# Kernel optimization log

Measured on AMD Instinct MI355X. Metric: run time of the kernel, lower is better.

## Reference

```python
import jax, jax.numpy as jnp
import numpy as np

# Config mirroring NEQUIPLayerFlax(hidden_irreps='64x0e + 64x1o', max_ell=1,
# avg_num_neighbors=16.0, num_species=5, mlp_n_hidden=64, mlp_n_layers=3, active_fn='relu')
N = 20000        # nodes
E = 320000       # edges (avg degree 16)
M = 64           # multiplicity per irrep
NR = 8           # radial embedding size
NSPEC = 5
AVG_NEI = 16.0
SQRT3 = 1.7320508075688772


def setup_inputs() -> dict:
    key = jax.random.key(0)
    ks = jax.random.split(key, 16)
    f32 = jnp.float32
    return {
        "vectors": jax.random.normal(ks[0], (E, 3), f32),
        "node_feats": jax.random.normal(ks[1], (N, 4 * M), f32),  # 64x0e (64) + 64x1o (192)
        "node_specie": jax.random.randint(ks[2], (N,), 0, NSPEC, jnp.int32),
        "radial_embedding": jax.random.uniform(ks[3], (E, NR), f32),
        "senders": jax.random.randint(ks[4], (E,), 0, N, jnp.int32),
        "receivers": jax.random.randint(ks[5], (E,), 0, N, jnp.int32),
        # linear_up: per-irrep-type mixing (no bias, e3nn-style /sqrt(fan_in))
        "W_up_s": jax.random.normal(ks[6], (M, M), f32),
        "W_up_v": jax.random.normal(ks[7], (M, M), f32),
        # radial MLP: NR -> 64 -> 64 -> 64 -> num_irreps(messages)=256
        "mlp_w1": jax.random.normal(ks[8], (NR, 64), f32),
        "mlp_w2": jax.random.normal(ks[9], (64, 64), f32),
        "mlp_w3": jax.random.normal(ks[10], (64, 64), f32),
        "mlp_wo": jax.random.normal(ks[11], (64, 4 * M), f32),
        # skip_tp: species-indexed linear node_feats -> (64x0e + 64x1o + 64x0e gates)
        "W_skip_s": jax.random.normal(ks[12], (NSPEC, M, 2 * M), f32),
        "W_skip_v": jax.random.normal(ks[13], (NSPEC, M, M), f32),
        # linear_down: messages (128x0e + 128x1o) -> (128x0e + 64x1o)
        "W_down_s": jax.random.normal(ks[14], (2 * M, 2 * M), f32),
        "W_down_v": jax.random.normal(ks[15], (2 * M, M), f32),
    }


def reference(vectors, node_feats, node_specie, radial_embedding, senders, receivers,
              W_up_s, W_up_v, mlp_w1, mlp_w2, mlp_w3, mlp_wo,
              W_skip_s, W_skip_v, W_down_s, W_down_v):
    n = node_feats.shape[0]
    s = node_feats[:, :M]                          # [N, 64]   0e
    v = node_feats[:, M:].reshape(n, M, 3)         # [N, 64,3] 1o

    inv_m = 1.0 / jnp.sqrt(jnp.asarray(M, node_feats.dtype))
    up_s = (s @ W_up_s) * inv_m                    # linear_up, scalar block
    up_v = jnp.einsum('nmc,mk->nkc', v, W_up_v) * inv_m

    es = up_s[senders]                             # [E, 64]
    ev = up_v[senders]                             # [E, 64, 3]

    # Y1 spherical harmonics, normalize=True, 'component' norm -> sqrt(3) * unit vector
    lengths = jnp.linalg.norm(vectors, axis=1, keepdims=True)         # [E,1]
    y = SQRT3 * vectors / lengths                                     # [E,3]

    # tensor products kept by filter_ir_out = hidden + '0e':
    # 1o x 1o -> 0e (CG = delta/sqrt(3), component norm)
    tp_s = jnp.einsum('emc,ec->em', ev, y) / SQRT3                    # [E,64]
    # 0e x 1o -> 1o (coefficient 1 under component norm)
    tp_v = es[:, :, None] * y[:, None, :]                             # [E,64,3]

    # concatenate + regroup -> 128x0e + 128x1o
    msg_s = jnp.concatenate([es, tp_s], axis=1)                       # [E,128]
    msg_v = jnp.concatenate([ev, tp_v], axis=1)                       # [E,128,3]

    # radial MLP (silu, /sqrt(fan_in) weight norm, no output activation)
    h = jax.nn.silu((radial_embedding @ mlp_w1) / jnp.sqrt(jnp.asarray(NR, jnp.float32)))
    h = jax.nn.silu((h @ mlp_w2) / 8.0)
    h = jax.nn.silu((h @ mlp_w3) / 8.0)
    mix = (h @ mlp_wo) / 8.0                                          # [E,256] = num_irreps
    mix = jnp.where(lengths == 0.0, 0.0, mix)

    msg_s = msg_s * mix[:, :2 * M]
    msg_v = msg_v * mix[:, 2 * M:, None]

    # scatter-sum to receivers, normalize by sqrt(avg_num_neighbors)
    inv_sq_nei = 1.0 / jnp.sqrt(jnp.asarray(AVG_NEI, jnp.float32))
    agg_s = jax.ops.segment_sum(msg_s, receivers, num_segments=n) * inv_sq_nei  # [N,128]
    agg_v = jax.ops.segment_sum(msg_v, receivers, num_segments=n) * inv_sq_nei  # [N,128,3]

    # linear_down -> irreps 64x0e + 64x1o + 64x0e(gates)  (scalars packed as 128)
    inv_2m = 1.0 / jnp.sqrt(jnp.asarray(2 * M, jnp.float32))
    down_s = (agg_s @ W_down_s) * inv_2m                              # [N,128]
    down_v = jnp.einsum('nmc,mk->nkc', agg_v, W_down_v) * inv_2m      # [N,64,3]

    # species-indexed skip connection from input node_feats
    Ws = W_skip_s[node_specie]                                        # [N,64,128]
    Wv = W_skip_v[node_specie]                                        # [N,64,64]
    skip_s = jnp.einsum('nm,nmk->nk', s, Ws) * inv_m                  # [N,128]
    skip_v = jnp.einsum('nmc,nmk->nkc', v, Wv) * inv_m                # [N,64,3]

    f_s = down_s + skip_s
    f_v = down_v + skip_v

    # gate: first 64 scalars are features (even_act=silu), last 64 scalars gate the 1o's
    gated_s = jax.nn.silu(f_s[:, :M])                                 # [N,64]
    gates = jax.nn.silu(f_s[:, M:])                                   # [N,64]
    gated_v = gates[:, :, None] * f_v                                 # [N,64,3]

    out = jnp.concatenate([gated_s, gated_v.reshape(n, 3 * M)], axis=1)  # [N,256]
    return jax.nn.relu(out)  # active_fn == 'relu'
```

## Files before the change

kernel.cpp:

```cpp
#include <hip/hip_runtime.h>
#include <hip/hip_fp16.h>

#define NN 20000
#define EE 320000
#define BCAP3 64

typedef _Float16 f16;
typedef f16  f16x8 __attribute__((ext_vector_type(8)));
typedef float f32x4 __attribute__((ext_vector_type(4)));

__device__ __forceinline__ float silu_f(float x) {
    return x / (1.0f + __expf(-x));
}

__global__ __launch_bounds__(256) void up_kernel(
    const float* __restrict__ nf, const float* __restrict__ Wus,
    const float* __restrict__ Wuv, float* __restrict__ up, int dmajor)
{
    __shared__ float sWs[64 * 64];
    __shared__ float sWv[64 * 64];
    int tid = threadIdx.x;
    for (int i = tid; i < 64 * 64; i += 256) { sWs[i] = Wus[i]; sWv[i] = Wuv[i]; }
    __syncthreads();
    int lane = tid & 63, wv = tid >> 6;
    for (int it = 0; it < 4; it++) {
        int n = blockIdx.x * 16 + wv * 4 + it;
        const float* row = nf + (size_t)n * 256;
        float s  = row[lane];
        float v0 = row[64 + lane * 3 + 0];
        float v1 = row[64 + lane * 3 + 1];
        float v2 = row[64 + lane * 3 + 2];
        float as = 0.f, a0 = 0.f, a1 = 0.f, a2 = 0.f;
        #pragma unroll 8
        for (int m = 0; m < 64; m++) {
            float sm = __shfl(s, m);
            float b0 = __shfl(v0, m), b1 = __shfl(v1, m), b2 = __shfl(v2, m);
            float w_s = sWs[m * 64 + lane];
            float w_v = sWv[m * 64 + lane];
            as += sm * w_s;
            a0 += b0 * w_v; a1 += b1 * w_v; a2 += b2 * w_v;
        }
        float* o = up + (size_t)n * 256;
        if (dmajor) {
            o[lane]       = as * 0.125f;
            o[64  + lane] = a0 * 0.125f;
            o[128 + lane] = a1 * 0.125f;
            o[192 + lane] = a2 * 0.125f;
        } else {
            o[lane] = as * 0.125f;
            o[64 + lane * 3 + 0] = a0 * 0.125f;
            o[64 + lane * 3 + 1] = a1 * 0.125f;
            o[64 + lane * 3 + 2] = a2 * 0.125f;
        }
    }
}

__global__ __launch_bounds__(256) void pack_kernel(
    const float* __restrict__ w1, const float* __restrict__ w2,
    const float* __restrict__ w3, const float* __restrict__ wo,
    f16* __restrict__ wp)
{
    int idx = blockIdx.x * 256 + threadIdx.x;
    if (idx >= 52 * 64) return;
    int frag = idx >> 6, lane = idx & 63;
    int col = lane & 15, kg = lane >> 4;
    f16x8 pv;
    if (frag < 4) {
        int t = frag;
        #pragma unroll
        for (int i = 0; i < 8; i++) {
            int k = kg * 8 + i;
            pv[i] = (k < 8) ? (f16)w1[k * 64 + t * 16 + col] : (f16)0.f;
        }
    } else if (frag < 12) {
        int f = frag - 4, t = f >> 1, h = f & 1;
        #pragma unroll
        for (int i = 0; i < 8; i++) {
            int k = h * 32 + kg * 8 + i;
            pv[i] = (f16)w2[k * 64 + t * 16 + col];
        }
    } else if (frag < 20) {
        int f = frag - 12, t = f >> 1, h = f & 1;
        #pragma unroll
        for (int i = 0; i < 8; i++) {
            int k = h * 32 + kg * 8 + i;
            pv[i] = (f16)w3[k * 64 + t * 16 + col];
        }
    } else {
        int f = frag - 20, t = f >> 1, h = f & 1;
        #pragma unroll
        for (int i = 0; i < 8; i++) {
            int k = h * 32 + kg * 8 + i;
            pv[i] = (f16)wo[k * 256 + t * 16 + col];
        }
    }
    *(f16x8*)(wp + (size_t)idx * 8) = pv;
}

__global__ __launch_bounds__(256) void pack2_kernel(
    const float* __restrict__ Wds, const float* __restrict__ Wdv,
    const float* __restrict__ Wss, const float* __restrict__ Wsv,
    f16* __restrict__ wp2)
{
    int idx = blockIdx.x * 256 + threadIdx.x;
    if (idx >= 168 * 64) return;
    int frag = idx >> 6, lane = idx & 63;
    int col = lane & 15, kg = lane >> 4;
    const float S_d = 0.25f * 0.08838834764831845f;
    const float S_k = 0.125f;
    f16x8 pv;
    if (frag < 32) {
        int t = frag >> 2, kf = frag & 3;
        #pragma unroll
        for (int i = 0; i < 8; i++) {
            int k = kf * 32 + kg * 8 + i;
            pv[i] = (f16)(Wds[k * 128 + t * 16 + col] * S_d);
        }
    } else if (frag < 48) {
        int f = frag - 32; int t = f >> 2, kf = f & 3;
        #pragma unroll
        for (int i = 0; i < 8; i++) {
            int k = kf * 32 + kg * 8 + i;
            pv[i] = (f16)(Wdv[k * 64 + t * 16 + col] * S_d);
        }
    } else if (frag < 128) {
        int f = frag - 48; int sp = f >> 4; int t = (f & 15) >> 1; int kf = f & 1;
        #pragma unroll
        for (int i = 0; i < 8; i++) {
            int k = kf * 32 + kg * 8 + i;
            pv[i] = (f16)(Wss[((size_t)sp * 64 + k) * 128 + t * 16 + col] * S_k);
        }
    } else {
        int f = frag - 128; int sp = f >> 3; int t = (f & 7) >> 1; int kf = f & 1;
        #pragma unroll
        for (int i = 0; i < 8; i++) {
            int k = kf * 32 + kg * 8 + i;
            pv[i] = (f16)(Wsv[((size_t)sp * 64 + k) * 64 + t * 16 + col] * S_k);
        }
    }
    *(f16x8*)(wp2 + (size_t)idx * 8) = pv;
}

__global__ void bucket_kernel(const int* __restrict__ rcv,
                              const int* __restrict__ snd,
                              int* __restrict__ cnt, int2* __restrict__ list)
{
    int e = blockIdx.x * 256 + threadIdx.x;
    int r = rcv[e];
    if ((unsigned)r >= (unsigned)NN) return;
    int s = snd[e];
    int pos = atomicAdd(&cnt[r], 1);
    if (pos < BCAP3) list[(size_t)r * BCAP3 + pos] = make_int2(e, s);
}

__global__ __launch_bounds__(256) void mlp_mix(
    const float* __restrict__ radial, const f16* __restrict__ wp,
    f16* __restrict__ mix)
{
    __shared__ f16 smem[4 * 6144];
    int tid = threadIdx.x, lane = tid & 63, w = tid >> 6;
    f16* actA = smem + w * 6144;
    f16* actB = actA + 1024;
    f16* outT = actB + 1024;
    int e0 = (blockIdx.x * 4 + w) * 16;

    int col = lane & 15;
    int kg  = lane >> 4;
    const f32x4 zero = {0.f, 0.f, 0.f, 0.f};

    #define LDB(fr) (*(const f16x8*)(wp + ((size_t)(fr) * 64 + lane) * 8))
    #define LDA(buf, h) (*(const f16x8*)((buf) + (lane & 15) * 64 + \
                        (((kg * 8) + (h) * 32) ^ (((lane & 15) & 7) << 3))))
    #define STACT(buf, acc, SC)                                            \
        _Pragma("unroll")                                                  \
        for (int t = 0; t < 4; t++) {                                      \
            _Pragma("unroll")                                              \
            for (int r = 0; r < 4; r++) {                                  \
                int row = kg * 4 + r;                                      \
                int c   = t * 16 + col;                                    \
                float x = acc[t][r] * (SC);                                \
                (buf)[row * 64 + (c ^ ((row & 7) << 3))] = (f16)silu_f(x); \
            }                                                              \
        }

    {
        f16x8 a;
        if (lane < 16) {
            const float* rr = radial + (size_t)(e0 + lane) * 8;
            float4 ra = *(const float4*)rr;
            float4 rb = *(const float4*)(rr + 4);
            a[0] = (f16)ra.x; a[1] = (f16)ra.y; a[2] = (f16)ra.z; a[3] = (f16)ra.w;
            a[4] = (f16)rb.x; a[5] = (f16)rb.y; a[6] = (f16)rb.z; a[7] = (f16)rb.w;
        } else {
            #pragma unroll
            for (int i = 0; i < 8; i++) a[i] = (f16)0.f;
        }
        f32x4 acc[4];
        #pragma unroll
        for (int t = 0; t < 4; t++)
            acc[t] = __builtin_amdgcn_mfma_f32_16x16x32_f16(a, LDB(t), zero, 0, 0, 0);
        STACT(actA, acc, 0.35355339059327373f)
    }
    {
        f16x8 a0 = LDA(actA, 0), a1 = LDA(actA, 1);
        f32x4 acc[4];
        #pragma unroll
        for (int t = 0; t < 4; t++) {
            acc[t] = __builtin_amdgcn_mfma_f32_16x16x32_f16(a0, LDB(4 + t * 2), zero, 0, 0, 0);
            acc[t] = __builtin_amdgcn_mfma_f32_16x16x32_f16(a1, LDB(5 + t * 2), acc[t], 0, 0, 0);
        }
        STACT(actB, acc, 0.125f)
    }
    {
        f16x8 a0 = LDA(actB, 0), a1 = LDA(actB, 1);
        f32x4 acc[4];
        #pragma unroll
        for (int t = 0; t < 4; t++) {
            acc[t] = __builtin_amdgcn_mfma_f32_16x16x32_f16(a0, LDB(12 + t * 2), zero, 0, 0, 0);
            acc[t] = __builtin_amdgcn_mfma_f32_16x16x32_f16(a1, LDB(13 + t * 2), acc[t], 0, 0, 0);
        }
        STACT(actA, acc, 0.125f)
    }
    {
        f16x8 a0 = LDA(actA, 0), a1 = LDA(actA, 1);
        #pragma unroll
        for (int tg = 0; tg < 4; tg++) {
            f32x4 acc[4];
            #pragma unroll
            for (int q = 0; q < 4; q++) {
                int t = tg * 4 + q;
                acc[q] = __builtin_amdgcn_mfma_f32_16x16x32_f16(a0, LDB(20 + t * 2), zero, 0, 0, 0);
                acc[q] = __builtin_amdgcn_mfma_f32_16x16x32_f16(a1, LDB(21 + t * 2), acc[q], 0, 0, 0);
            }
            #pragma unroll
            for (int q = 0; q < 4; q++) {
                int t = tg * 4 + q;
                #pragma unroll
                for (int r = 0; r < 4; r++) {
                    int row = kg * 4 + r;
                    int c   = t * 16 + col;
                    outT[row * 256 + (c ^ ((row & 7) << 3))] = (f16)(acc[q][r] * 0.125f);
                }
            }
        }
    }
    #pragma unroll
    for (int j = 0; j < 8; j++) {
        int li  = j * 64 + lane;
        int row = li >> 5;
        int ci  = (li & 31) * 8;
        f16x8 v = *(const f16x8*)(outT + row * 256 + (ci ^ ((row & 7) << 3)));
        *(f16x8*)(mix + (size_t)(e0 + row) * 256 + ci) = v;
    }
    #undef LDB
    #undef LDA
    #undef STACT
}

__global__ __launch_bounds__(256) void gather_kernel(
    const float* __restrict__ vectors,
    const f16* __restrict__ mix, const float* __restrict__ up2,
    const int* __restrict__ cnt, const int2* __restrict__ list,
    f16* __restrict__ agg)
{
    int tid = threadIdx.x, lane = tid & 63, w = tid >> 6;
    int n = blockIdx.x * 4 + w;
    if ((unsigned)n >= (unsigned)NN) return;
    int count = cnt[n];
    if (count > BCAP3) count = BCAP3;
    if (count < 0) count = 0;

    int sec = lane >> 3;
    int m0  = (lane & 7) * 8;
    int upoff = (sec == 2) ? 64 + m0 : (sec == 3) ? 128 + m0
              : (sec == 4) ? 192 + m0 : m0;
    int mq = (sec == 0) ? 0 : (sec == 1) ? 64 : (sec <= 4) ? 128 : 192;
    const float SQ3 = 1.7320508075688772f;

    float a0=0,a1=0,a2=0,a3=0,a4=0,a5=0,a6=0,a7=0;
    const int2* mylist = list + (size_t)n * BCAP3;

    for (int k = 0; k < count; k++) {
        int2 es = mylist[k];
        int e   = es.x;
        int snd = es.y;
        if ((unsigned)e >= (unsigned)EE) e = 0;
        if ((unsigned)snd >= (unsigned)NN) snd = 0;
        float vx = vectors[(size_t)e * 3 + 0];
        float vy = vectors[(size_t)e * 3 + 1];
        float vz = vectors[(size_t)e * 3 + 2];
        float l2 = vx * vx + vy * vy + vz * vz;
        float il   = (l2 > 0.f) ? rsqrtf(l2) : 0.f;
        float mask = (l2 > 0.f) ? 1.f : 0.f;

        f16x8 mv = *(const f16x8*)(mix + (size_t)e * 256 + mq + m0);
        const float* u = up2 + (size_t)snd * 256;

        if (sec != 1) {
            float g = (sec == 5) ? SQ3 * vx * il
                    : (sec == 6) ? SQ3 * vy * il
                    : (sec == 7) ? SQ3 * vz * il : mask;
            const float* ub = u + upoff;
            float4 u0 = *(const float4*)(ub);
            float4 u1 = *(const float4*)(ub + 4);
            a0 += u0.x * g * (float)mv[0];
            a1 += u0.y * g * (float)mv[1];
            a2 += u0.z * g * (float)mv[2];
            a3 += u0.w * g * (float)mv[3];
            a4 += u1.x * g * (float)mv[4];
            a5 += u1.y * g * (float)mv[5];
            a6 += u1.z * g * (float)mv[6];
            a7 += u1.w * g * (float)mv[7];
        } else {
            float4 ex0 = *(const float4*)(u + 64  + m0);
            float4 ex1 = *(const float4*)(u + 64  + m0 + 4);
            float4 ey0 = *(const float4*)(u + 128 + m0);
            float4 ey1 = *(const float4*)(u + 128 + m0 + 4);
            float4 ez0 = *(const float4*)(u + 192 + m0);
            float4 ez1 = *(const float4*)(u + 192 + m0 + 4);
            a0 += (ex0.x * vx + ey0.x * vy + ez0.x * vz) * il * (float)mv[0];
            a1 += (ex0.y * vx + ey0.y * vy + ez0.y * vz) * il * (float)mv[1];
            a2 += (ex0.z * vx + ey0.z * vy + ez0.z * vz) * il * (float)mv[2];
            a3 += (ex0.w * vx + ey0.w * vy + ez0.w * vz) * il * (float)mv[3];
            a4 += (ex1.x * vx + ey1.x * vy + ez1.x * vz) * il * (float)mv[4];
            a5 += (ex1.y * vx + ey1.y * vy + ez1.y * vz) * il * (float)mv[5];
            a6 += (ex1.z * vx + ey1.z * vy + ez1.z * vz) * il * (float)mv[6];
            a7 += (ex1.w * vx + ey1.w * vy + ez1.w * vz) * il * (float)mv[7];
        }
    }
    f16x8 o;
    o[0] = (f16)a0; o[1] = (f16)a1; o[2] = (f16)a2; o[3] = (f16)a3;
    o[4] = (f16)a4; o[5] = (f16)a5; o[6] = (f16)a6; o[7] = (f16)a7;
    *(f16x8*)(agg + (size_t)n * 512 + lane * 8) = o;
}

__global__ __launch_bounds__(256) void node_mfma(
    const float* __restrict__ nf, const int* __restrict__ specie,
    const f16* __restrict__ wp2, const f16* __restrict__ agg,
    float* __restrict__ out)
{
    int tid = threadIdx.x, lane = tid & 63, w = tid >> 6;
    int n0 = (blockIdx.x * 4 + w) * 16;
    if (n0 >= NN) return;
    int col = lane & 15, kg = lane >> 4;
    int myn = n0 + col;
    int mysp = specie[myn];
    if ((unsigned)mysp >= 5u) mysp = 0;
    const f32x4 zero = {0.f, 0.f, 0.f, 0.f};
    const f16x8 zv = {};

    #define LDB2(fr) (*(const f16x8*)(wp2 + ((size_t)(fr) * 64 + lane) * 8))

    f32x4 accs[8];
    #pragma unroll
    for (int t = 0; t < 8; t++) accs[t] = zero;
    #pragma unroll
    for (int kf = 0; kf < 4; kf++) {
        f16x8 a = *(const f16x8*)(agg + (size_t)myn * 512 + kf * 32 + kg * 8);
        #pragma unroll
        for (int t = 0; t < 8; t++)
            accs[t] = __builtin_amdgcn_mfma_f32_16x16x32_f16(a, LDB2(t * 4 + kf), accs[t], 0, 0, 0);
    }
    #pragma unroll
    for (int kf = 0; kf < 2; kf++) {
        const float* base = nf + (size_t)myn * 256 + kf * 32 + kg * 8;
        float4 x0 = *(const float4*)(base);
        float4 x1 = *(const float4*)(base + 4);
        f16x8 a;
        a[0] = (f16)x0.x; a[1] = (f16)x0.y; a[2] = (f16)x0.z; a[3] = (f16)x0.w;
        a[4] = (f16)x1.x; a[5] = (f16)x1.y; a[6] = (f16)x1.z; a[7] = (f16)x1.w;
        #pragma unroll
        for (int sp = 0; sp < 5; sp++) {
            f16x8 am = (mysp == sp) ? a : zv;
            #pragma unroll
            for (int t = 0; t < 8; t++)
                accs[t] = __builtin_amdgcn_mfma_f32_16x16x32_f16(am, LDB2(48 + sp * 16 + t * 2 + kf), accs[t], 0, 0, 0);
        }
    }
    float gates[4][4];
    #pragma unroll
    for (int t = 0; t < 4; t++) {
        #pragma unroll
        for (int r = 0; r < 4; r++) {
            int n = n0 + kg * 4 + r;
            out[(size_t)n * 256 + t * 16 + col] = fmaxf(silu_f(accs[t][r]), 0.f);
            gates[t][r] = silu_f(accs[4 + t][r]);
        }
    }

    #pragma unroll
    for (int c = 0; c < 3; c++) {
        f32x4 accv[4];
        #pragma unroll
        for (int t = 0; t < 4; t++) accv[t] = zero;
        #pragma unroll
        for (int kf = 0; kf < 4; kf++) {
            int off = (kf < 2) ? (128 + c * 64 + kf * 32) : (320 + c * 64 + (kf - 2) * 32);
            f16x8 a = *(const f16x8*)(agg + (size_t)myn * 512 + off + kg * 8);
            #pragma unroll
            for (int t = 0; t < 4; t++)
                accv[t] = __builtin_amdgcn_mfma_f32_16x16x32_f16(a, LDB2(32 + t * 4 + kf), accv[t], 0, 0, 0);
        }
        #pragma unroll
        for (int kf = 0; kf < 2; kf++) {
            const float* base = nf + (size_t)myn * 256 + 64 + (kf * 32 + kg * 8) * 3;
            float4 q0 = *(const float4*)(base);
            float4 q1 = *(const float4*)(base + 4);
            float4 q2 = *(const float4*)(base + 8);
            float4 q3 = *(const float4*)(base + 12);
            float4 q4 = *(const float4*)(base + 16);
            float4 q5 = *(const float4*)(base + 20);
            float qa[24] = {q0.x, q0.y, q0.z, q0.w, q1.x, q1.y, q1.z, q1.w,
                            q2.x, q2.y, q2.z, q2.w, q3.x, q3.y, q3.z, q3.w,
                            q4.x, q4.y, q4.z, q4.w, q5.x, q5.y, q5.z, q5.w};
            f16x8 a;
            #pragma unroll
            for (int i = 0; i < 8; i++) a[i] = (f16)qa[i * 3 + c];
            #pragma unroll
            for (int sp = 0; sp < 5; sp++) {
                f16x8 am = (mysp == sp) ? a : zv;
                #pragma unroll
                for (int t = 0; t < 4; t++)
                    accv[t] = __builtin_amdgcn_mfma_f32_16x16x32_f16(am, LDB2(128 + sp * 8 + t * 2 + kf), accv[t], 0, 0, 0);
            }
        }
        #pragma unroll
        for (int t = 0; t < 4; t++) {
            #pragma unroll
            for (int r = 0; r < 4; r++) {
                int n = n0 + kg * 4 + r;
                out[(size_t)n * 256 + 64 + (t * 16 + col) * 3 + c] =
                    fmaxf(gates[t][r] * accv[t][r], 0.f);
            }
        }
    }
    #undef LDB2
}

__global__ __launch_bounds__(256) void node_kernel_f(
    const float* __restrict__ nf, const int* __restrict__ specie,
    const float* __restrict__ Wds, const float* __restrict__ Wdv,
    const float* __restrict__ Wss, const float* __restrict__ Wsv,
    const float* __restrict__ agg, float* __restrict__ out)
{
    __shared__ float sDs[128 * 128];
    __shared__ float sDv[128 * 64];
    int tid = threadIdx.x;
    for (int i = tid; i < 128 * 128; i += 256) sDs[i] = Wds[i];
    for (int i = tid; i < 128 * 64; i += 256) sDv[i] = Wdv[i];
    __syncthreads();
    int lane = tid & 63, wv = tid >> 6;
    for (int it = 0; it < 4; it++) {
        int n = blockIdx.x * 16 + wv * 4 + it;
        const float* arow = agg + (size_t)n * 512;
        const float inv_nei = 0.25f;
        float as0 = arow[lane] * inv_nei;
        float as1 = arow[64 + lane] * inv_nei;
        float av00 = arow[128 + lane] * inv_nei;
        float av01 = arow[192 + lane] * inv_nei;
        float av02 = arow[256 + lane] * inv_nei;
        float av10 = arow[320 + lane] * inv_nei;
        float av11 = arow[384 + lane] * inv_nei;
        float av12 = arow[448 + lane] * inv_nei;
        const float* row = nf + (size_t)n * 256;
        float s   = row[lane];
        float vv0 = row[64 + lane * 3 + 0];
        float vv1 = row[64 + lane * 3 + 1];
        float vv2 = row[64 + lane * 3 + 2];

        float f0 = 0.f, f1 = 0.f, fv0 = 0.f, fv1 = 0.f, fv2 = 0.f;
        #pragma unroll 8
        for (int m = 0; m < 64; m++) {
            float am = __shfl(as0, m);
            f0 += am * sDs[m * 128 + lane];
            f1 += am * sDs[m * 128 + 64 + lane];
            float b0 = __shfl(av00, m), b1 = __shfl(av01, m), b2 = __shfl(av02, m);
            float wd = sDv[m * 64 + lane];
            fv0 += b0 * wd; fv1 += b1 * wd; fv2 += b2 * wd;
        }
        #pragma unroll 8
        for (int m = 0; m < 64; m++) {
            float am = __shfl(as1, m);
            f0 += am * sDs[(64 + m) * 128 + lane];
            f1 += am * sDs[(64 + m) * 128 + 64 + lane];
            float b0 = __shfl(av10, m), b1 = __shfl(av11, m), b2 = __shfl(av12, m);
            float wd = sDv[(64 + m) * 64 + lane];
            fv0 += b0 * wd; fv1 += b1 * wd; fv2 += b2 * wd;
        }
        const float inv2m = 0.08838834764831845f;
        f0 *= inv2m; f1 *= inv2m; fv0 *= inv2m; fv1 *= inv2m; fv2 *= inv2m;

        int sp = specie[n];
        if ((unsigned)sp >= 5u) sp = 0;
        const float* Ws = Wss + (size_t)sp * 64 * 128;
        const float* Wv = Wsv + (size_t)sp * 64 * 64;
        float g0 = 0.f, g1 = 0.f, h0 = 0.f, h1 = 0.f, h2 = 0.f;
        #pragma unroll 4
        for (int m = 0; m < 64; m++) {
            float sm = __shfl(s, m);
            g0 += sm * Ws[m * 128 + lane];
            g1 += sm * Ws[m * 128 + 64 + lane];
            float b0 = __shfl(vv0, m), b1 = __shfl(vv1, m), b2 = __shfl(vv2, m);
            float wsk = Wv[m * 64 + lane];
            h0 += b0 * wsk; h1 += b1 * wsk; h2 += b2 * wsk;
        }
        f0 += g0 * 0.125f; f1 += g1 * 0.125f;
        fv0 += h0 * 0.125f; fv1 += h1 * 0.125f; fv2 += h2 * 0.125f;

        float gs   = silu_f(f0);
        float gate = silu_f(f1);
        float* orow = out + (size_t)n * 256;
        orow[lane] = fmaxf(gs, 0.f);
        orow[64 + lane * 3 + 0] = fmaxf(gate * fv0, 0.f);
        orow[64 + lane * 3 + 1] = fmaxf(gate * fv1, 0.f);
        orow[64 + lane * 3 + 2] = fmaxf(gate * fv2, 0.f);
    }
}

__global__ __launch_bounds__(256) void edge_kernel_fb(
    const float* __restrict__ vectors, const float* __restrict__ radial,
    const int* __restrict__ senders, const int* __restrict__ receivers,
    const float* __restrict__ w1, const float* __restrict__ w2,
    const float* __restrict__ w3, const float* __restrict__ wo,
    const float* __restrict__ up, float* __restrict__ agg)
{
    __shared__ __half2 hL[32 * 256];
    __shared__ float   T[16 * 256];
    __shared__ float   sVec[256 * 3];
    __shared__ int     sSnd[256];
    __shared__ int     sRcv[256];

    int tid = threadIdx.x;
    int e = blockIdx.x * 256 + tid;
    int snd = senders[e];
    int rcv = receivers[e];
    if ((unsigned)snd >= (unsigned)NN) snd = 0;
    if ((unsigned)rcv >= (unsigned)NN) rcv = 0;
    float4 ra = *(const float4*)(radial + (size_t)e * 8);
    float4 rb = *(const float4*)(radial + (size_t)e * 8 + 4);
    float vx = vectors[(size_t)e * 3 + 0];
    float vy = vectors[(size_t)e * 3 + 1];
    float vz = vectors[(size_t)e * 3 + 2];
    sSnd[tid] = snd; sRcv[tid] = rcv;
    sVec[tid * 3 + 0] = vx; sVec[tid * 3 + 1] = vy; sVec[tid * 3 + 2] = vz;
    float len2 = vx * vx + vy * vy + vz * vz;
    float mask = (len2 > 0.f) ? 1.f : 0.f;

    {
        float a[64];
        #pragma unroll
        for (int j = 0; j < 64; j++) {
            float acc = ra.x * w1[j]       + ra.y * w1[64 + j]
                      + ra.z * w1[128 + j] + ra.w * w1[192 + j]
                      + rb.x * w1[256 + j] + rb.y * w1[320 + j]
                      + rb.z * w1[384 + j] + rb.w * w1[448 + j];
            a[j] = silu_f(acc * 0.35355339059327373f);
        }
        #pragma unroll
        for (int jp = 0; jp < 32; jp++)
            hL[jp * 256 + tid] = __floats2half2_rn(a[2 * jp], a[2 * jp + 1]);
    }
    {
        float acc[64];
        #pragma unroll
        for (int j = 0; j < 64; j++) acc[j] = 0.f;
        #pragma unroll 2
        for (int kp = 0; kp < 32; kp++) {
            float2 hf = __half22float2(hL[kp * 256 + tid]);
            const float* wr0 = w2 + (size_t)(2 * kp) * 64;
            const float* wr1 = w2 + (size_t)(2 * kp + 1) * 64;
            #pragma unroll
            for (int j = 0; j < 64; j++) acc[j] += hf.x * wr0[j] + hf.y * wr1[j];
        }
        #pragma unroll
        for (int jp = 0; jp < 32; jp++)
            hL[jp * 256 + tid] = __floats2half2_rn(silu_f(acc[2 * jp] * 0.125f),
                                                   silu_f(acc[2 * jp + 1] * 0.125f));
    }
    {
        float acc[64];
        #pragma unroll
        for (int j = 0; j < 64; j++) acc[j] = 0.f;
        #pragma unroll 2
        for (int kp = 0; kp < 32; kp++) {
            float2 hf = __half22float2(hL[kp * 256 + tid]);
            const float* wr0 = w3 + (size_t)(2 * kp) * 64;
            const float* wr1 = w3 + (size_t)(2 * kp + 1) * 64;
            #pragma unroll
            for (int j = 0; j < 64; j++) acc[j] += hf.x * wr0[j] + hf.y * wr1[j];
        }
        #pragma unroll
        for (int jp = 0; jp < 32; jp++)
            hL[jp * 256 + tid] = __floats2half2_rn(silu_f(acc[2 * jp] * 0.125f),
                                                   silu_f(acc[2 * jp + 1] * 0.125f));
    }

    int lane  = tid & 63;
    int wbase = tid & 192;
    int f = lane & 15;
    int g = lane >> 4;

    #define COMPUTE_CHUNK(c, ao)                                                \
        {                                                                       \
            _Pragma("unroll")                                                   \
            for (int j = 0; j < 16; j++) ao[j] = 0.f;                           \
            _Pragma("unroll 4")                                                 \
            for (int kp = 0; kp < 32; kp++) {                                   \
                float2 hf = __half22float2(hL[kp * 256 + tid]);                 \
                const float* wr0 = wo + (size_t)(2 * kp) * 256 + (c) * 16;      \
                const float* wr1 = wo + (size_t)(2 * kp + 1) * 256 + (c) * 16;  \
                _Pragma("unroll")                                               \
                for (int j = 0; j < 16; j++)                                    \
                    ao[j] += hf.x * wr0[j] + hf.y * wr1[j];                     \
            }                                                                   \
            _Pragma("unroll")                                                   \
            for (int j = 0; j < 16; j++) ao[j] *= 0.125f * mask;                \
        }

    #define WRITE_T(ao)                                                         \
        __syncthreads();                                                        \
        _Pragma("unroll")                                                       \
        for (int j = 0; j < 16; j++) T[j * 256 + (tid ^ (2 * j))] = ao[j];      \
        __syncthreads();

    for (int c = 0; c < 4; c++) {
        float ao[16];
        COMPUTE_CHUNK(c, ao)
        WRITE_T(ao)
        for (int el = 0; el < 16; el++) {
            int col = wbase + el * 4 + g;
            int s_ = sSnd[col], rc = sRcv[col];
            float mx = T[f * 256 + (col ^ (2 * f))];
            int jf = c * 16 + f;
            atomicAdd(agg + (size_t)rc * 512 + jf, up[(size_t)s_ * 256 + jf] * mx);
        }
    }
    for (int c = 4; c < 8; c++) {
        float ao[16];
        COMPUTE_CHUNK(c, ao)
        WRITE_T(ao)
        for (int el = 0; el < 16; el++) {
            int col = wbase + el * 4 + g;
            int s_ = sSnd[col], rc = sRcv[col];
            float wx = sVec[col * 3 + 0], wy = sVec[col * 3 + 1], wz = sVec[col * 3 + 2];
            float l2 = wx * wx + wy * wy + wz * wz;
            float il = (l2 > 0.f) ? rsqrtf(l2) : 0.f;
            float mx = T[f * 256 + (col ^ (2 * f))];
            int m = (c - 4) * 16 + f;
            const float* ev = up + (size_t)s_ * 256 + 64 + m * 3;
            float dot = ev[0] * wx + ev[1] * wy + ev[2] * wz;
            atomicAdd(agg + (size_t)rc * 512 + 64 + m, dot * il * mx);
        }
    }
    for (int c = 8; c < 12; c++) {
        float ao[16];
        COMPUTE_CHUNK(c, ao)
        WRITE_T(ao)
        for (int el = 0; el < 16; el++) {
            int col = wbase + el * 4 + g;
            int s_ = sSnd[col], rc = sRcv[col];
            float mx = T[f * 256 + (col ^ (2 * f))];
            int m = (c - 8) * 16 + f;
            const float* ev = up + (size_t)s_ * 256 + 64 + m * 3;
            float* ag = agg + (size_t)rc * 512 + 128 + m;
            atomicAdd(ag + 0,   ev[0] * mx);
            atomicAdd(ag + 64,  ev[1] * mx);
            atomicAdd(ag + 128, ev[2] * mx);
        }
    }
    for (int c = 12; c < 16; c++) {
        float ao[16];
        COMPUTE_CHUNK(c, ao)
        WRITE_T(ao)
        for (int el = 0; el < 16; el++) {
            int col = wbase + el * 4 + g;
            int s_ = sSnd[col], rc = sRcv[col];
            float wx = sVec[col * 3 + 0], wy = sVec[col * 3 + 1], wz = sVec[col * 3 + 2];
            float l2 = wx * wx + wy * wy + wz * wz;
            float il = (l2 > 0.f) ? rsqrtf(l2) : 0.f;
            float mx = T[f * 256 + (col ^ (2 * f))];
            int m = (c - 12) * 16 + f;
            float sc = up[(size_t)s_ * 256 + m] * 1.7320508075688772f * il * mx;
            float* ag = agg + (size_t)rc * 512 + 320 + m;
            atomicAdd(ag + 0,   sc * wx);
            atomicAdd(ag + 64,  sc * wy);
            atomicAdd(ag + 128, sc * wz);
        }
    }
    #undef COMPUTE_CHUNK
    #undef WRITE_T
}

extern "C" void kernel_launch(void* const* d_in, const int* in_sizes, int n_in,
                              void* d_out, int out_size, void* d_ws, size_t ws_size,
                              hipStream_t stream) {
    const float* vectors     = (const float*)d_in[0];
    const float* node_feats  = (const float*)d_in[1];
    const int*   node_specie = (const int*)d_in[2];
    const float* radial      = (const float*)d_in[3];
    const int*   senders     = (const int*)d_in[4];
    const int*   receivers   = (const int*)d_in[5];
    const float* W_up_s      = (const float*)d_in[6];
    const float* W_up_v      = (const float*)d_in[7];
    const float* mlp_w1      = (const float*)d_in[8];
    const float* mlp_w2      = (const float*)d_in[9];
    const float* mlp_w3      = (const float*)d_in[10];
    const float* mlp_wo      = (const float*)d_in[11];
    const float* W_skip_s    = (const float*)d_in[12];
    const float* W_skip_v    = (const float*)d_in[13];
    const float* W_down_s    = (const float*)d_in[14];
    const float* W_down_v    = (const float*)d_in[15];
    float* out = (float*)d_out;

    float* up   = (float*)d_ws;
    float* aggf = up + (size_t)NN * 256;
    f16*   aggh = (f16*)aggf;
    int*   cnt  = (int*)((char*)aggf + 21 * 1024 * 1024);
    int2*  list = (int2*)(cnt + 20480);
    uintptr_t wp_addr = ((uintptr_t)(aggf + (size_t)NN * 512) + 255) & ~(uintptr_t)255;
    f16* wpack = (f16*)wp_addr;
    f16* wp2   = wpack + (size_t)52 * 64 * 8;
    uintptr_t mix_addr = ((uintptr_t)(wp2 + (size_t)168 * 64 * 8) + 255) & ~(uintptr_t)255;
    f16* mix = (f16*)mix_addr;
    size_t required = (size_t)(mix_addr + (size_t)EE * 256 * sizeof(f16)
                               - (uintptr_t)d_ws);

    if (ws_size >= required) {
        hipMemsetAsync(cnt, 0, NN * sizeof(int), stream);
        pack_kernel<<<13, 256, 0, stream>>>(mlp_w1, mlp_w2, mlp_w3, mlp_wo, wpack);
        pack2_kernel<<<42, 256, 0, stream>>>(W_down_s, W_down_v, W_skip_s, W_skip_v, wp2);
        up_kernel<<<NN / 16, 256, 0, stream>>>(node_feats, W_up_s, W_up_v, up, 1);
        bucket_kernel<<<EE / 256, 256, 0, stream>>>(receivers, senders, cnt, list);
        mlp_mix<<<EE / 64, 256, 0, stream>>>(radial, wpack, mix);
        gather_kernel<<<NN / 4, 256, 0, stream>>>(vectors, mix, up,
            cnt, list, aggh);
        node_mfma<<<(NN / 16 + 3) / 4, 256, 0, stream>>>(node_feats, node_specie,
            wp2, aggh, out);
    } else {
        hipMemsetAsync(aggf, 0, (size_t)NN * 512 * sizeof(float), stream);
        up_kernel<<<NN / 16, 256, 0, stream>>>(node_feats, W_up_s, W_up_v, up, 0);
        edge_kernel_fb<<<EE / 256, 256, 0, stream>>>(
            vectors, radial, senders, receivers,
            mlp_w1, mlp_w2, mlp_w3, mlp_wo, up, aggf);
        node_kernel_f<<<NN / 16, 256, 0, stream>>>(node_feats, node_specie,
            W_down_s, W_down_v, W_skip_s, W_skip_v, aggf, out);
    }
}
```

Baseline: 324.2 us.

## Sort edges by receiver via CSR scan so gather reads mix contiguously

Adds a prefix-sum over per-receiver counts and a slot-map kernel that produces receiver-sorted edge order, then runs the edge MLP in that order so the per-edge mix rows for each node are stored contiguously. The gather kernel reads its messages sequentially instead of from scattered edge rows, improving locality on the large fp16 mix buffer. It adds a single-block scan and a scatter kernel, and moves the random access to the small radial rows.

```diff
diff --git a/kernel.cpp b/kernel.cpp
--- a/kernel.cpp
+++ b/kernel.cpp
@@ -153,16 +153,58 @@
     if (pos < BCAP3) list[(size_t)r * BCAP3 + pos] = make_int2(e, s);
 }
 
+__global__ __launch_bounds__(256) void scan_kernel(
+    const int* __restrict__ cnt, int* __restrict__ off)
+{
+    __shared__ int partial[256];
+    int t = threadIdx.x;
+    int base = t * 79;
+    int end  = base + 79; if (end > NN) end = NN; if (base > NN) base = NN;
+    int sum = 0;
+    for (int i = base; i < end; i++) {
+        int c = cnt[i]; if (c > BCAP3) c = BCAP3; if (c < 0) c = 0;
+        sum += c;
+    }
+    partial[t] = sum;
+    __syncthreads();
+    for (int d = 1; d < 256; d <<= 1) {
+        int v = (t >= d) ? partial[t - d] : 0;
+        __syncthreads();
+        partial[t] += v;
+        __syncthreads();
+    }
+    int run = (t == 0) ? 0 : partial[t - 1];
+    for (int i = base; i < end; i++) {
+        int c = cnt[i]; if (c > BCAP3) c = BCAP3; if (c < 0) c = 0;
+        off[i] = run;
+        run += c;
+    }
+}
+
+__global__ __launch_bounds__(256) void slotmap_kernel(
+    const int* __restrict__ cnt, const int* __restrict__ off,
+    const int2* __restrict__ list, int2* __restrict__ slotEs)
+{
+    int idx = blockIdx.x * 256 + threadIdx.x;
+    int n = idx >> 6, k = idx & 63;
+    if (n >= NN) return;
+    int c = cnt[n]; if (c > BCAP3) c = BCAP3; if (c < 0) c = 0;
+    if (k >= c) return;
+    int pos = off[n] + k;
+    if ((unsigned)pos < (unsigned)EE)
+        slotEs[pos] = list[(size_t)n * BCAP3 + k];
+}
+
 __global__ __launch_bounds__(256) void mlp_mix(
     const float* __restrict__ radial, const f16* __restrict__ wp,
-    f16* __restrict__ mix)
+    const int2* __restrict__ slotEs, f16* __restrict__ mix)
 {
     __shared__ f16 smem[4 * 6144];
     int tid = threadIdx.x, lane = tid & 63, w = tid >> 6;
     f16* actA = smem + w * 6144;
     f16* actB = actA + 1024;
     f16* outT = actB + 1024;
-    int e0 = (blockIdx.x * 4 + w) * 16;
+    int s0 = (blockIdx.x * 4 + w) * 16;
 
     int col = lane & 15;
     int kg  = lane >> 4;
@@ -186,7 +228,9 @@
     {
         f16x8 a;
         if (lane < 16) {
-            const float* rr = radial + (size_t)(e0 + lane) * 8;
+            int e = slotEs[s0 + lane].x;
+            if ((unsigned)e >= (unsigned)EE) e = 0;
+            const float* rr = radial + (size_t)e * 8;
             float4 ra = *(const float4*)rr;
             float4 rb = *(const float4*)(rr + 4);
             a[0] = (f16)ra.x; a[1] = (f16)ra.y; a[2] = (f16)ra.z; a[3] = (f16)ra.w;
@@ -250,7 +294,7 @@
         int row = li >> 5;
         int ci  = (li & 31) * 8;
         f16x8 v = *(const f16x8*)(outT + row * 256 + (ci ^ ((row & 7) << 3)));
-        *(f16x8*)(mix + (size_t)(e0 + row) * 256 + ci) = v;
+        *(f16x8*)(mix + (size_t)(s0 + row) * 256 + ci) = v;
     }
     #undef LDB
     #undef LDA
@@ -260,8 +304,8 @@
 __global__ __launch_bounds__(256) void gather_kernel(
     const float* __restrict__ vectors,
     const f16* __restrict__ mix, const float* __restrict__ up2,
-    const int* __restrict__ cnt, const int2* __restrict__ list,
-    f16* __restrict__ agg)
+    const int* __restrict__ cnt, const int* __restrict__ off,
+    const int2* __restrict__ slotEs, f16* __restrict__ agg)
 {
     int tid = threadIdx.x, lane = tid & 63, w = tid >> 6;
     int n = blockIdx.x * 4 + w;
@@ -269,6 +313,10 @@
     int count = cnt[n];
     if (count > BCAP3) count = BCAP3;
     if (count < 0) count = 0;
+    int o = off[n];
+    if (o < 0) o = 0;
+    if (o > EE) o = EE;
+    if (o + count > EE) count = EE - o;
 
     int sec = lane >> 3;
     int m0  = (lane & 7) * 8;
@@ -278,7 +326,8 @@
     const float SQ3 = 1.7320508075688772f;
 
     float a0=0,a1=0,a2=0,a3=0,a4=0,a5=0,a6=0,a7=0;
-    const int2* mylist = list + (size_t)n * BCAP3;
+    const int2* mylist = slotEs + o;
+    const f16*  mybase = mix + (size_t)o * 256;
 
     for (int k = 0; k < count; k++) {
         int2 es = mylist[k];
@@ -293,7 +342,7 @@
         float il   = (l2 > 0.f) ? rsqrtf(l2) : 0.f;
         float mask = (l2 > 0.f) ? 1.f : 0.f;
 
-        f16x8 mv = *(const f16x8*)(mix + (size_t)e * 256 + mq + m0);
+        f16x8 mv = *(const f16x8*)(mybase + (size_t)k * 256 + mq + m0);
         const float* u = up2 + (size_t)snd * 256;
 
         if (sec != 1) {
@@ -328,10 +377,10 @@
             a7 += (ex1.w * vx + ey1.w * vy + ez1.w * vz) * il * (float)mv[7];
         }
     }
-    f16x8 o;
-    o[0] = (f16)a0; o[1] = (f16)a1; o[2] = (f16)a2; o[3] = (f16)a3;
-    o[4] = (f16)a4; o[5] = (f16)a5; o[6] = (f16)a6; o[7] = (f16)a7;
-    *(f16x8*)(agg + (size_t)n * 512 + lane * 8) = o;
+    f16x8 oo;
+    oo[0] = (f16)a0; oo[1] = (f16)a1; oo[2] = (f16)a2; oo[3] = (f16)a3;
+    oo[4] = (f16)a4; oo[5] = (f16)a5; oo[6] = (f16)a6; oo[7] = (f16)a7;
+    *(f16x8*)(agg + (size_t)n * 512 + lane * 8) = oo;
 }
 
 __global__ __launch_bounds__(256) void node_mfma(
@@ -395,8 +444,8 @@
         for (int t = 0; t < 4; t++) accv[t] = zero;
         #pragma unroll
         for (int kf = 0; kf < 4; kf++) {
-            int off = (kf < 2) ? (128 + c * 64 + kf * 32) : (320 + c * 64 + (kf - 2) * 32);
-            f16x8 a = *(const f16x8*)(agg + (size_t)myn * 512 + off + kg * 8);
+            int off2 = (kf < 2) ? (128 + c * 64 + kf * 32) : (320 + c * 64 + (kf - 2) * 32);
+            f16x8 a = *(const f16x8*)(agg + (size_t)myn * 512 + off2 + kg * 8);
             #pragma unroll
             for (int t = 0; t < 4; t++)
                 accv[t] = __builtin_amdgcn_mfma_f32_16x16x32_f16(a, LDB2(32 + t * 4 + kf), accv[t], 0, 0, 0);
@@ -716,7 +765,9 @@
     float* aggf = up + (size_t)NN * 256;
     f16*   aggh = (f16*)aggf;
     int*   cnt  = (int*)((char*)aggf + 21 * 1024 * 1024);
-    int2*  list = (int2*)(cnt + 20480);
+    int*   offs = cnt + 20480;
+    int2*  slotEs = (int2*)(offs + 20480);
+    int2*  list = slotEs + EE;
     uintptr_t wp_addr = ((uintptr_t)(aggf + (size_t)NN * 512) + 255) & ~(uintptr_t)255;
     f16* wpack = (f16*)wp_addr;
     f16* wp2   = wpack + (size_t)52 * 64 * 8;
@@ -731,9 +782,11 @@
         pack2_kernel<<<42, 256, 0, stream>>>(W_down_s, W_down_v, W_skip_s, W_skip_v, wp2);
         up_kernel<<<NN / 16, 256, 0, stream>>>(node_feats, W_up_s, W_up_v, up, 1);
         bucket_kernel<<<EE / 256, 256, 0, stream>>>(receivers, senders, cnt, list);
-        mlp_mix<<<EE / 64, 256, 0, stream>>>(radial, wpack, mix);
+        scan_kernel<<<1, 256, 0, stream>>>(cnt, offs);
+        slotmap_kernel<<<NN * 64 / 256, 256, 0, stream>>>(cnt, offs, list, slotEs);
+        mlp_mix<<<EE / 64, 256, 0, stream>>>(radial, wpack, slotEs, mix);
         gather_kernel<<<NN / 4, 256, 0, stream>>>(vectors, mix, up,
-            cnt, list, aggh);
+            cnt, offs, slotEs, aggh);
         node_mfma<<<(NN / 16 + 3) / 4, 256, 0, stream>>>(node_feats, node_specie,
             wp2, aggh, out);
     } else {
```

Result: slower. 367.7 us (+13.4%).

## Fuse radial MLP into per-receiver gather, drop edge mix buffer

Applied to the files above, without the earlier changes.

Merges the per-edge radial MLP kernel and the receiver gather kernel into one. Each wavefront now takes up to 16 of its node's incoming edges at a time, runs the MLP on them with MFMA, keeps the 256-wide mixing weights in shared memory, and accumulates messages straight from there. This removes writing and re-reading the E×256 fp16 mix buffer, about 160MB of traffic each way. In exchange, MLP tiles are only partly filled when a node has fewer than 16 or an awkward number of neighbours, and the edge-wise MLP is now serialised with the gather inside each wave.

```diff
diff --git a/kernel.cpp b/kernel.cpp
--- a/kernel.cpp
+++ b/kernel.cpp
@@ -153,185 +153,177 @@
     if (pos < BCAP3) list[(size_t)r * BCAP3 + pos] = make_int2(e, s);
 }
 
-__global__ __launch_bounds__(256) void mlp_mix(
+__global__ __launch_bounds__(256) void mlp_gather2(
     const float* __restrict__ radial, const f16* __restrict__ wp,
-    f16* __restrict__ mix)
+    const float* __restrict__ vectors, const float* __restrict__ up2,
+    const int* __restrict__ cnt, const int2* __restrict__ list,
+    f16* __restrict__ agg)
 {
-    __shared__ f16 smem[4 * 6144];
+    __shared__ f16 smem[4 * 5120];
     int tid = threadIdx.x, lane = tid & 63, w = tid >> 6;
-    f16* actA = smem + w * 6144;
-    f16* actB = actA + 1024;
-    f16* outT = actB + 1024;
-    int e0 = (blockIdx.x * 4 + w) * 16;
-
-    int col = lane & 15;
-    int kg  = lane >> 4;
+    f16* actA = smem + w * 5120;
+    f16* outT = actA + 1024;
+    int n = blockIdx.x * 4 + w;
+    if ((unsigned)n >= (unsigned)NN) return;
+    int count = cnt[n];
+    if (count > BCAP3) count = BCAP3;
+    if (count < 0) count = 0;
+
+    int col = lane & 15, kg = lane >> 4;
     const f32x4 zero = {0.f, 0.f, 0.f, 0.f};
+    const float SQ3 = 1.7320508075688772f;
+
+    int sec = lane >> 3;
+    int m0  = (lane & 7) * 8;
+    int upoff = (sec == 2) ? 64 + m0 : (sec == 3) ? 128 + m0
+              : (sec == 4) ? 192 + m0 : m0;
+    int mq = (sec == 0) ? 0 : (sec == 1) ? 64 : (sec <= 4) ? 128 : 192;
+    float a0=0,a1=0,a2=0,a3=0,a4=0,a5=0,a6=0,a7=0;
+
+    const int2* mylist = list + (size_t)n * BCAP3;
 
     #define LDB(fr) (*(const f16x8*)(wp + ((size_t)(fr) * 64 + lane) * 8))
     #define LDA(buf, h) (*(const f16x8*)((buf) + (lane & 15) * 64 + \
                         (((kg * 8) + (h) * 32) ^ (((lane & 15) & 7) << 3))))
-    #define STACT(buf, acc, SC)                                            \
+    #define STACT(buf, a4v, SC)                                            \
         _Pragma("unroll")                                                  \
         for (int t = 0; t < 4; t++) {                                      \
             _Pragma("unroll")                                              \
             for (int r = 0; r < 4; r++) {                                  \
                 int row = kg * 4 + r;                                      \
                 int c   = t * 16 + col;                                    \
-                float x = acc[t][r] * (SC);                                \
+                float x = a4v[t][r] * (SC);                                \
                 (buf)[row * 64 + (c ^ ((row & 7) << 3))] = (f16)silu_f(x); \
             }                                                              \
         }
 
-    {
-        f16x8 a;
-        if (lane < 16) {
-            const float* rr = radial + (size_t)(e0 + lane) * 8;
-            float4 ra = *(const float4*)rr;
-            float4 rb = *(const float4*)(rr + 4);
-            a[0] = (f16)ra.x; a[1] = (f16)ra.y; a[2] = (f16)ra.z; a[3] = (f16)ra.w;
-            a[4] = (f16)rb.x; a[5] = (f16)rb.y; a[6] = (f16)rb.z; a[7] = (f16)rb.w;
-        } else {
-            #pragma unroll
-            for (int i = 0; i < 8; i++) a[i] = (f16)0.f;
-        }
-        f32x4 acc[4];
-        #pragma unroll
-        for (int t = 0; t < 4; t++)
-            acc[t] = __builtin_amdgcn_mfma_f32_16x16x32_f16(a, LDB(t), zero, 0, 0, 0);
-        STACT(actA, acc, 0.35355339059327373f)
-    }
-    {
-        f16x8 a0 = LDA(actA, 0), a1 = LDA(actA, 1);
-        f32x4 acc[4];
-        #pragma unroll
-        for (int t = 0; t < 4; t++) {
-            acc[t] = __builtin_amdgcn_mfma_f32_16x16x32_f16(a0, LDB(4 + t * 2), zero, 0, 0, 0);
-            acc[t] = __builtin_amdgcn_mfma_f32_16x16x32_f16(a1, LDB(5 + t * 2), acc[t], 0, 0, 0);
-        }
-        STACT(actB, acc, 0.125f)
-    }
-    {
-        f16x8 a0 = LDA(actB, 0), a1 = LDA(actB, 1);
-        f32x4 acc[4];
-        #pragma unroll
-        for (int t = 0; t < 4; t++) {
-            acc[t] = __builtin_amdgcn_mfma_f32_16x16x32_f16(a0, LDB(12 + t * 2), zero, 0, 0, 0);
-            acc[t] = __builtin_amdgcn_mfma_f32_16x16x32_f16(a1, LDB(13 + t * 2), acc[t], 0, 0, 0);
-        }
-        STACT(actA, acc, 0.125f)
-    }
-    {
-        f16x8 a0 = LDA(actA, 0), a1 = LDA(actA, 1);
-        #pragma unroll
-        for (int tg = 0; tg < 4; tg++) {
-            f32x4 acc[4];
-            #pragma unroll
-            for (int q = 0; q < 4; q++) {
-                int t = tg * 4 + q;
-                acc[q] = __builtin_amdgcn_mfma_f32_16x16x32_f16(a0, LDB(20 + t * 2), zero, 0, 0, 0);
-                acc[q] = __builtin_amdgcn_mfma_f32_16x16x32_f16(a1, LDB(21 + t * 2), acc[q], 0, 0, 0);
+    for (int base = 0; base < count; base += 16) {
+        int2 es = make_int2(0, 0);
+        bool valid = (lane < 16) && (base + lane < count);
+        if (valid) es = mylist[base + lane];
+
+        {
+            f16x8 a;
+            if (valid) {
+                int e = es.x;
+                if ((unsigned)e >= (unsigned)EE) e = 0;
+                const float* rr = radial + (size_t)e * 8;
+                float4 ra = *(const float4*)rr;
+                float4 rb = *(const float4*)(rr + 4);
+                a[0] = (f16)ra.x; a[1] = (f16)ra.y; a[2] = (f16)ra.z; a[3] = (f16)ra.w;
+                a[4] = (f16)rb.x; a[5] = (f16)rb.y; a[6] = (f16)rb.z; a[7] = (f16)rb.w;
+            } else {
+                #pragma unroll
+                for (int i = 0; i < 8; i++) a[i] = (f16)0.f;
             }
-            #pragma unroll
-            for (int q = 0; q < 4; q++) {
-                int t = tg * 4 + q;
+            f32x4 av[4];
+            #pragma unroll
+            for (int t = 0; t < 4; t++)
+                av[t] = __builtin_amdgcn_mfma_f32_16x16x32_f16(a, LDB(t), zero, 0, 0, 0);
+            STACT(actA, av, 0.35355339059327373f)
+        }
+        {
+            f16x8 q0 = LDA(actA, 0), q1 = LDA(actA, 1);
+            f32x4 av[4];
+            #pragma unroll
+            for (int t = 0; t < 4; t++) {
+                av[t] = __builtin_amdgcn_mfma_f32_16x16x32_f16(q0, LDB(4 + t * 2), zero, 0, 0, 0);
+                av[t] = __builtin_amdgcn_mfma_f32_16x16x32_f16(q1, LDB(5 + t * 2), av[t], 0, 0, 0);
+            }
+            STACT(actA, av, 0.125f)
+        }
+        {
+            f16x8 q0 = LDA(actA, 0), q1 = LDA(actA, 1);
+            f32x4 av[4];
+            #pragma unroll
+            for (int t = 0; t < 4; t++) {
+                av[t] = __builtin_amdgcn_mfma_f32_16x16x32_f16(q0, LDB(12 + t * 2), zero, 0, 0, 0);
+                av[t] = __builtin_amdgcn_mfma_f32_16x16x32_f16(q1, LDB(13 + t * 2), av[t], 0, 0, 0);
+            }
+            STACT(actA, av, 0.125f)
+        }
+        {
+            f16x8 q0 = LDA(actA, 0), q1 = LDA(actA, 1);
+            #pragma unroll
+            for (int tg = 0; tg < 4; tg++) {
+                f32x4 av[4];
                 #pragma unroll
-                for (int r = 0; r < 4; r++) {
-                    int row = kg * 4 + r;
-                    int c   = t * 16 + col;
-                    outT[row * 256 + (c ^ ((row & 7) << 3))] = (f16)(acc[q][r] * 0.125f);
+                for (int q = 0; q < 4; q++) {
+                    int t = tg * 4 + q;
+                    av[q] = __builtin_amdgcn_mfma_f32_16x16x32_f16(q0, LDB(20 + t * 2), zero, 0, 0, 0);
+                    av[q] = __builtin_amdgcn_mfma_f32_16x16x32_f16(q1, LDB(21 + t * 2), av[q], 0, 0, 0);
+                }
+                #pragma unroll
+                for (int q = 0; q < 4; q++) {
+                    int t = tg * 4 + q;
+                    #pragma unroll
+                    for (int r = 0; r < 4; r++) {
+                        int row = kg * 4 + r;
+                        int c   = t * 16 + col;
+                        outT[row * 256 + (c ^ ((row & 7) << 3))] = (f16)(av[q][r] * 0.125f);
+                    }
                 }
             }
         }
-    }
-    #pragma unroll
-    for (int j = 0; j < 8; j++) {
-        int li  = j * 64 + lane;
-        int row = li >> 5;
-        int ci  = (li & 31) * 8;
-        f16x8 v = *(const f16x8*)(outT + row * 256 + (ci ^ ((row & 7) << 3)));
-        *(f16x8*)(mix + (size_t)(e0 + row) * 256 + ci) = v;
+
+        int nel = count - base; if (nel > 16) nel = 16;
+        for (int el = 0; el < nel; el++) {
+            int e   = __shfl(es.x, el);
+            int snd = __shfl(es.y, el);
+            if ((unsigned)e >= (unsigned)EE) e = 0;
+            if ((unsigned)snd >= (unsigned)NN) snd = 0;
+            float vx = vectors[(size_t)e * 3 + 0];
+            float vy = vectors[(size_t)e * 3 + 1];
+            float vz = vectors[(size_t)e * 3 + 2];
+            float l2 = vx * vx + vy * vy + vz * vz;
+            float il   = (l2 > 0.f) ? rsqrtf(l2) : 0.f;
+            float mask = (l2 > 0.f) ? 1.f : 0.f;
+
+            int sw = (el & 7) << 3;
+            f16x8 mv = *(const f16x8*)(outT + el * 256 + ((mq + m0) ^ sw));
+            const float* u = up2 + (size_t)snd * 256;
+
+            if (sec != 1) {
+                float g = (sec == 5) ? SQ3 * vx * il
+                        : (sec == 6) ? SQ3 * vy * il
+                        : (sec == 7) ? SQ3 * vz * il : mask;
+                const float* ub = u + upoff;
+                float4 u0 = *(const float4*)(ub);
+                float4 u1 = *(const float4*)(ub + 4);
+                a0 += u0.x * g * (float)mv[0];
+                a1 += u0.y * g * (float)mv[1];
+                a2 += u0.z * g * (float)mv[2];
+                a3 += u0.w * g * (float)mv[3];
+                a4 += u1.x * g * (float)mv[4];
+                a5 += u1.y * g * (float)mv[5];
+                a6 += u1.z * g * (float)mv[6];
+                a7 += u1.w * g * (float)mv[7];
+            } else {
+                float4 ex0 = *(const float4*)(u + 64  + m0);
+                float4 ex1 = *(const float4*)(u + 64  + m0 + 4);
+                float4 ey0 = *(const float4*)(u + 128 + m0);
+                float4 ey1 = *(const float4*)(u + 128 + m0 + 4);
+                float4 ez0 = *(const float4*)(u + 192 + m0);
+                float4 ez1 = *(const float4*)(u + 192 + m0 + 4);
+                a0 += (ex0.x * vx + ey0.x * vy + ez0.x * vz) * il * (float)mv[0];
+                a1 += (ex0.y * vx + ey0.y * vy + ez0.y * vz) * il * (float)mv[1];
+                a2 += (ex0.z * vx + ey0.z * vy + ez0.z * vz) * il * (float)mv[2];
+                a3 += (ex0.w * vx + ey0.w * vy + ez0.w * vz) * il * (float)mv[3];
+                a4 += (ex1.x * vx + ey1.x * vy + ez1.x * vz) * il * (float)mv[4];
+                a5 += (ex1.y * vx + ey1.y * vy + ez1.y * vz) * il * (float)mv[5];
+                a6 += (ex1.z * vx + ey1.z * vy + ez1.z * vz) * il * (float)mv[6];
+                a7 += (ex1.w * vx + ey1.w * vy + ez1.w * vz) * il * (float)mv[7];
+            }
+        }
     }
     #undef LDB
     #undef LDA
     #undef STACT
-}
-
-__global__ __launch_bounds__(256) void gather_kernel(
-    const float* __restrict__ vectors,
-    const f16* __restrict__ mix, const float* __restrict__ up2,
-    const int* __restrict__ cnt, const int2* __restrict__ list,
-    f16* __restrict__ agg)
-{
-    int tid = threadIdx.x, lane = tid & 63, w = tid >> 6;
-    int n = blockIdx.x * 4 + w;
-    if ((unsigned)n >= (unsigned)NN) return;
-    int count = cnt[n];
-    if (count > BCAP3) count = BCAP3;
-    if (count < 0) count = 0;
-
-    int sec = lane >> 3;
-    int m0  = (lane & 7) * 8;
-    int upoff = (sec == 2) ? 64 + m0 : (sec == 3) ? 128 + m0
-              : (sec == 4) ? 192 + m0 : m0;
-    int mq = (sec == 0) ? 0 : (sec == 1) ? 64 : (sec <= 4) ? 128 : 192;
-    const float SQ3 = 1.7320508075688772f;
-
-    float a0=0,a1=0,a2=0,a3=0,a4=0,a5=0,a6=0,a7=0;
-    const int2* mylist = list + (size_t)n * BCAP3;
-
-    for (int k = 0; k < count; k++) {
-        int2 es = mylist[k];
-        int e   = es.x;
-        int snd = es.y;
-        if ((unsigned)e >= (unsigned)EE) e = 0;
-        if ((unsigned)snd >= (unsigned)NN) snd = 0;
-        float vx = vectors[(size_t)e * 3 + 0];
-        float vy = vectors[(size_t)e * 3 + 1];
-        float vz = vectors[(size_t)e * 3 + 2];
-        float l2 = vx * vx + vy * vy + vz * vz;
-        float il   = (l2 > 0.f) ? rsqrtf(l2) : 0.f;
-        float mask = (l2 > 0.f) ? 1.f : 0.f;
-
-        f16x8 mv = *(const f16x8*)(mix + (size_t)e * 256 + mq + m0);
-        const float* u = up2 + (size_t)snd * 256;
-
-        if (sec != 1) {
-            float g = (sec == 5) ? SQ3 * vx * il
-                    : (sec == 6) ? SQ3 * vy * il
-                    : (sec == 7) ? SQ3 * vz * il : mask;
-            const float* ub = u + upoff;
-            float4 u0 = *(const float4*)(ub);
-            float4 u1 = *(const float4*)(ub + 4);
-            a0 += u0.x * g * (float)mv[0];
-            a1 += u0.y * g * (float)mv[1];
-            a2 += u0.z * g * (float)mv[2];
-            a3 += u0.w * g * (float)mv[3];
-            a4 += u1.x * g * (float)mv[4];
-            a5 += u1.y * g * (float)mv[5];
-            a6 += u1.z * g * (float)mv[6];
-            a7 += u1.w * g * (float)mv[7];
-        } else {
-            float4 ex0 = *(const float4*)(u + 64  + m0);
-            float4 ex1 = *(const float4*)(u + 64  + m0 + 4);
-            float4 ey0 = *(const float4*)(u + 128 + m0);
-            float4 ey1 = *(const float4*)(u + 128 + m0 + 4);
-            float4 ez0 = *(const float4*)(u + 192 + m0);
-            float4 ez1 = *(const float4*)(u + 192 + m0 + 4);
-            a0 += (ex0.x * vx + ey0.x * vy + ez0.x * vz) * il * (float)mv[0];
-            a1 += (ex0.y * vx + ey0.y * vy + ez0.y * vz) * il * (float)mv[1];
-            a2 += (ex0.z * vx + ey0.z * vy + ez0.z * vz) * il * (float)mv[2];
-            a3 += (ex0.w * vx + ey0.w * vy + ez0.w * vz) * il * (float)mv[3];
-            a4 += (ex1.x * vx + ey1.x * vy + ez1.x * vz) * il * (float)mv[4];
-            a5 += (ex1.y * vx + ey1.y * vy + ez1.y * vz) * il * (float)mv[5];
-            a6 += (ex1.z * vx + ey1.z * vy + ez1.z * vz) * il * (float)mv[6];
-            a7 += (ex1.w * vx + ey1.w * vy + ez1.w * vz) * il * (float)mv[7];
-        }
-    }
-    f16x8 o;
-    o[0] = (f16)a0; o[1] = (f16)a1; o[2] = (f16)a2; o[3] = (f16)a3;
-    o[4] = (f16)a4; o[5] = (f16)a5; o[6] = (f16)a6; o[7] = (f16)a7;
-    *(f16x8*)(agg + (size_t)n * 512 + lane * 8) = o;
+
+    f16x8 oo;
+    oo[0] = (f16)a0; oo[1] = (f16)a1; oo[2] = (f16)a2; oo[3] = (f16)a3;
+    oo[4] = (f16)a4; oo[5] = (f16)a5; oo[6] = (f16)a6; oo[7] = (f16)a7;
+    *(f16x8*)(agg + (size_t)n * 512 + lane * 8) = oo;
 }
 
 __global__ __launch_bounds__(256) void node_mfma(
@@ -395,8 +387,8 @@
         for (int t = 0; t < 4; t++) accv[t] = zero;
         #pragma unroll
         for (int kf = 0; kf < 4; kf++) {
-            int off = (kf < 2) ? (128 + c * 64 + kf * 32) : (320 + c * 64 + (kf - 2) * 32);
-            f16x8 a = *(const f16x8*)(agg + (size_t)myn * 512 + off + kg * 8);
+            int off2 = (kf < 2) ? (128 + c * 64 + kf * 32) : (320 + c * 64 + (kf - 2) * 32);
+            f16x8 a = *(const f16x8*)(agg + (size_t)myn * 512 + off2 + kg * 8);
             #pragma unroll
             for (int t = 0; t < 4; t++)
                 accv[t] = __builtin_amdgcn_mfma_f32_16x16x32_f16(a, LDB2(32 + t * 4 + kf), accv[t], 0, 0, 0);
@@ -720,9 +712,7 @@
     uintptr_t wp_addr = ((uintptr_t)(aggf + (size_t)NN * 512) + 255) & ~(uintptr_t)255;
     f16* wpack = (f16*)wp_addr;
     f16* wp2   = wpack + (size_t)52 * 64 * 8;
-    uintptr_t mix_addr = ((uintptr_t)(wp2 + (size_t)168 * 64 * 8) + 255) & ~(uintptr_t)255;
-    f16* mix = (f16*)mix_addr;
-    size_t required = (size_t)(mix_addr + (size_t)EE * 256 * sizeof(f16)
+    size_t required = (size_t)((uintptr_t)(wp2 + (size_t)168 * 64 * 8)
                                - (uintptr_t)d_ws);
 
     if (ws_size >= required) {
@@ -731,8 +721,7 @@
         pack2_kernel<<<42, 256, 0, stream>>>(W_down_s, W_down_v, W_skip_s, W_skip_v, wp2);
         up_kernel<<<NN / 16, 256, 0, stream>>>(node_feats, W_up_s, W_up_v, up, 1);
         bucket_kernel<<<EE / 256, 256, 0, stream>>>(receivers, senders, cnt, list);
-        mlp_mix<<<EE / 64, 256, 0, stream>>>(radial, wpack, mix);
-        gather_kernel<<<NN / 4, 256, 0, stream>>>(vectors, mix, up,
+        mlp_gather2<<<NN / 4, 256, 0, stream>>>(radial, wpack, vectors, up,
             cnt, list, aggh);
         node_mfma<<<(NN / 16 + 3) / 4, 256, 0, stream>>>(node_feats, node_specie,
             wp2, aggh, out);
```

Result: slower. 731.9 us (+125.8%).
